# Kernel tuning notes

Hardware: AMD Instinct MI355X
Metric: run time of the kernel (lower is better)

The kernel has to match this reference:

```python
import jax, jax.numpy as jnp
import numpy as np
import math

N_ITERS = 10
N_SPIXELS = 256
NEG_INF = -1e10


def _grid_layout(h, w, n_spixels):
    # init_grid: near-square superpixel grid
    nw = int(math.sqrt(n_spixels * w / h))
    nh = int(math.sqrt(n_spixels * h / w))
    cy = np.minimum((np.arange(h) * nh) // h, nh - 1)
    cx = np.minimum((np.arange(w) * nw) // w, nw - 1)
    iy = np.broadcast_to(cy[:, None], (h, w))
    ix = np.broadcast_to(cx[None, :], (h, w))
    init_idx = iy * nw + ix  # [h,w] hard grid assignment
    # 9 candidate superpixels per pixel (3x3 neighborhood of its grid cell)
    offs = np.array([(dy, dx) for dy in (-1, 0, 1) for dx in (-1, 0, 1)])
    ny = iy[None] + offs[:, 0, None, None]  # [9,h,w]
    nx = ix[None] + offs[:, 1, None, None]
    valid = (ny >= 0) & (ny < nh) & (nx >= 0) & (nx < nw)
    nidx = np.clip(ny, 0, nh - 1) * nw + np.clip(nx, 0, nw - 1)
    return init_idx.astype(np.int32), nidx.astype(np.int32), valid, nw, nh


def setup_inputs() -> dict:
    key = jax.random.key(0)
    x = jax.random.normal(key, (2, 20, 512, 512), dtype=jnp.float32)
    return {"x": x}


def reference(x):
    b, c, h, w = x.shape
    init_idx_np, nidx_np, valid_np, nw, nh = _grid_layout(h, w, N_SPIXELS)
    K = nw * nh
    n = h * w
    init_idx = jnp.asarray(init_idx_np.reshape(n))          # [N]
    nidx = jnp.asarray(nidx_np.reshape(9, n))                # [9,N]
    valid = jnp.asarray(valid_np.reshape(9, n))              # [9,N]
    flat_nidx = nidx.reshape(-1)                             # [9N]

    pf_all = x.reshape(b, c, n)

    def init_spf(pf):  # pf [c,N] -> [c,K]: hard-assignment mean (InitSpixelFeats)
        s = jax.ops.segment_sum(pf.T, init_idx, num_segments=K)      # [K,c]
        cnt = jax.ops.segment_sum(jnp.ones((n,), pf.dtype), init_idx, num_segments=K)
        return (s / jnp.maximum(cnt, 1.0)[:, None]).T

    def calc_neg_dist(pf, spf):  # CalcAssoc: [9,N] neg sq dist to 9 neighbors
        nf = spf[:, nidx]                                    # [c,9,N]
        d = jnp.sum((pf[:, None, :] - nf) ** 2, axis=0)      # [9,N]
        return jnp.where(valid, -d, NEG_INF)

    def map_p2sp(pf, Q):  # CalcSpixelFeats: Q-weighted scatter mean, Q [9,N]
        wf = (pf[:, None, :] * Q[None]).reshape(c, -1)       # [c,9N]
        num = jax.ops.segment_sum(wf.T, flat_nidx, num_segments=K)   # [K,c]
        den = jax.ops.segment_sum(Q.reshape(-1), flat_nidx, num_segments=K)
        return (num / jnp.maximum(den, 1e-8)[:, None]).T

    def per_sample(pf):
        spf0 = init_spf(jax.lax.stop_gradient(pf))  # spf init from detached pf
        Q0 = jnp.zeros((9, n), pf.dtype)
        def body(carry, _):
            spf, _ = carry
            Q = jax.nn.softmax(calc_neg_dist(pf, spf), axis=0)
            return (map_p2sp(pf, Q), Q), None
        (spf, Q), _ = jax.lax.scan(body, (spf0, Q0), None, length=N_ITERS)
        return Q, spf

    Q, spf = jax.vmap(per_sample)(pf_all)
    return Q.reshape(b, 9, h, w), spf, x
```

## Files before the change

### kernel.cpp

```cpp
#include <hip/hip_runtime.h>

#define BATCH 2
#define C 20
#define H 512
#define W 512
#define NPIX (H*W)
#define NW 16
#define NH 16
#define K 256
#define NITERS 10
#define SPLIT 4
#define PITCH 260
#define NEG_INF_F (-1.0e10f)
#define PART_STRIDE 189

__global__ void ssn_init_kernel(const float* __restrict__ x,
                                float* __restrict__ spf0) {
    int bi = blockIdx.x;
    int ch = bi % C;
    int k  = (bi / C) % K;
    int b  = bi / (C * K);
    int ky = k >> 4, kx = k & 15;
    const float* src = x + ((size_t)(b * C + ch)) * NPIX;
    int l = threadIdx.x;
    float s = 0.f;
#pragma unroll
    for (int i = 0; i < 16; ++i) {
        int p = l + 64 * i;
        int y = ky * 32 + (p >> 5);
        int xx = kx * 32 + (p & 31);
        s += src[y * W + xx];
    }
#pragma unroll
    for (int o = 32; o > 0; o >>= 1) s += __shfl_down(s, o);
    if (l == 0) spf0[(b * K + k) * C + ch] = s * (1.0f / 1024.0f);
}

__global__ void ssn_reduce_kernel(const float* __restrict__ part,
                                  float* __restrict__ spf,
                                  float* __restrict__ outSpf,
                                  int final_mode) {
    int idx = blockIdx.x * blockDim.x + threadIdx.x;
    if (idx >= BATCH * K * C) return;
    int ch = idx % C;
    int k  = (idx / C) % K;
    int b  = idx / (C * K);
    int ky = k >> 4, kx = k & 15;
    float num = 0.f, den = 0.f;
#pragma unroll
    for (int j2 = 0; j2 < 9; ++j2) {
        int cy = ky - (j2 / 3 - 1), cx = kx - (j2 % 3 - 1);
        if (cy >= 0 && cy < NH && cx >= 0 && cx < NW) {
            const float* p = part +
                (size_t)(b * K + cy * NW + cx) * (SPLIT * PART_STRIDE) + j2 * 21;
#pragma unroll
            for (int ss = 0; ss < SPLIT; ++ss) {
                num += p[ss * PART_STRIDE + ch];
                den += p[ss * PART_STRIDE + 20];
            }
        }
    }
    float v = num / fmaxf(den, 1e-8f);
    if (final_mode) outSpf[(b * C + ch) * K + k] = v;
    else            spf[(b * K + k) * C + ch]    = v;
}

__global__ __launch_bounds__(256)
void ssn_iterate_kernel(const float* __restrict__ x,
                        const float* __restrict__ spf,
                        float* __restrict__ wpart,
                        float* __restrict__ outQ,
                        int last) {
    __shared__ float spf_lds[9][C];
    __shared__ float sumsq_lds[9];
    __shared__ float pf_tile[C][PITCH];
    __shared__ float w_tile[9][PITCH];

    int t = threadIdx.x;
    int bi = blockIdx.x;
    int s    = bi & 3;
    int cell = (bi >> 2) & (K - 1);
    int b    = bi >> 10;
    int ky = cell >> 4, kx = cell & 15;

    if (t < 9 * C) {
        int jj = t / C, ch = t % C;
        int ny = ky + jj / 3 - 1, nx = kx + jj % 3 - 1;
        float v = 0.f;
        if (ny >= 0 && ny < NH && nx >= 0 && nx < NW)
            v = spf[(size_t)(b * K + ny * NW + nx) * C + ch];
        spf_lds[jj][ch] = v;
    }
    if (t < 9) {
        int ny = ky + t / 3 - 1, nx = kx + t % 3 - 1;
        float ss2 = 0.f;
        if (ny >= 0 && ny < NH && nx >= 0 && nx < NW) {
            const float* sp = spf + (size_t)(b * K + ny * NW + nx) * C;
#pragma unroll
            for (int ch = 0; ch < C; ++ch) ss2 += sp[ch] * sp[ch];
        }
        sumsq_lds[t] = ss2;
    }
    __syncthreads();

    int py = t >> 5, px = t & 31;
    int y  = ky * 32 + s * 8 + py;
    int xx = kx * 32 + px;

    float pf[C];
    const float* xb = x + (size_t)b * C * NPIX + y * W + xx;
#pragma unroll
    for (int ch = 0; ch < C; ++ch) pf[ch] = xb[(size_t)ch * NPIX];

    float sc[9];
#pragma unroll
    for (int j = 0; j < 9; ++j) {
        int ny = ky + j / 3 - 1, nx = kx + j % 3 - 1;
        bool valid = (ny >= 0 && ny < NH && nx >= 0 && nx < NW);
        float dot = 0.f;
#pragma unroll
        for (int ch = 0; ch < C; ++ch) dot = fmaf(pf[ch], spf_lds[j][ch], dot);
        sc[j] = valid ? fmaf(2.f, dot, -sumsq_lds[j]) : NEG_INF_F;
    }
    float m = sc[0];
#pragma unroll
    for (int j = 1; j < 9; ++j) m = fmaxf(m, sc[j]);
    float wv[9], wsum = 0.f;
#pragma unroll
    for (int j = 0; j < 9; ++j) { wv[j] = __expf(sc[j] - m); wsum += wv[j]; }
    float inv = 1.0f / wsum;
#pragma unroll
    for (int j = 0; j < 9; ++j) { wv[j] *= inv; w_tile[j][t] = wv[j]; }
#pragma unroll
    for (int ch = 0; ch < C; ++ch) pf_tile[ch][t] = pf[ch];

    if (last) {
        float* q = outQ + (size_t)b * 9 * NPIX + y * W + xx;
#pragma unroll
        for (int j = 0; j < 9; ++j) q[(size_t)j * NPIX] = wv[j];
    }
    __syncthreads();

    if (t < PART_STRIDE) {
        int j = t / 21, r = t % 21;
        const float4* wt = (const float4*)&w_tile[j][0];
        float acc = 0.f;
        if (r < 20) {
            const float4* pt = (const float4*)&pf_tile[r][0];
#pragma unroll 4
            for (int p = 0; p < 64; ++p) {
                float4 w4 = wt[p];
                float4 f4 = pt[p];
                acc += w4.x * f4.x + w4.y * f4.y + w4.z * f4.z + w4.w * f4.w;
            }
        } else {
#pragma unroll 4
            for (int p = 0; p < 64; ++p) {
                float4 w4 = wt[p];
                acc += w4.x + w4.y + w4.z + w4.w;
            }
        }
        wpart[(size_t)(b * K + cell) * (SPLIT * PART_STRIDE)
              + s * PART_STRIDE + t] = acc;
    }
}

extern "C" void kernel_launch(void* const* d_in, const int* in_sizes, int n_in,
                              void* d_out, int out_size, void* d_ws, size_t ws_size,
                              hipStream_t stream) {
    const float* x = (const float*)d_in[0];
    float* out = (float*)d_out;
    float* outQ   = out;
    float* outSpf = out + (size_t)BATCH * 9 * NPIX;
    float* outX   = outSpf + (size_t)BATCH * C * K;

    float* ws   = (float*)d_ws;
    float* spf  = ws;
    float* part = spf + (size_t)BATCH * K * C;

    hipMemcpyAsync(outX, x, sizeof(float) * (size_t)BATCH * C * NPIX,
                   hipMemcpyDeviceToDevice, stream);

    ssn_init_kernel<<<BATCH * K * C, 64, 0, stream>>>(x, spf);

    for (int it = 0; it < NITERS; ++it) {
        ssn_iterate_kernel<<<BATCH * K * SPLIT, 256, 0, stream>>>(
            x, spf, part, outQ, (it == NITERS - 1) ? 1 : 0);
        if (it < NITERS - 1)
            ssn_reduce_kernel<<<(BATCH * K * C + 255) / 256, 256, 0, stream>>>(
                part, spf, nullptr, 0);
    }
    ssn_reduce_kernel<<<(BATCH * K * C + 255) / 256, 256, 0, stream>>>(
        part, nullptr, outSpf, 1);
}
```

Measured before the change: 273.1 us.

## Fuse x copy into init, register-tile the weighted scatter reduction, hoist pixel loads

```diff
diff --git a/kernel.cpp b/kernel.cpp
--- a/kernel.cpp
+++ b/kernel.cpp
@@ -14,26 +14,55 @@
 #define NEG_INF_F (-1.0e10f)
 #define PART_STRIDE 189
 
-__global__ void ssn_init_kernel(const float* __restrict__ x,
-                                float* __restrict__ spf0) {
+__global__ __launch_bounds__(256)
+void ssn_init_kernel(const float* __restrict__ x,
+                     float* __restrict__ outX,
+                     float* __restrict__ wpart) {
+    __shared__ float pf_tile[C][PITCH];
+    __shared__ float chpart[80];
+    int t = threadIdx.x;
     int bi = blockIdx.x;
-    int ch = bi % C;
-    int k  = (bi / C) % K;
-    int b  = bi / (C * K);
-    int ky = k >> 4, kx = k & 15;
-    const float* src = x + ((size_t)(b * C + ch)) * NPIX;
-    int l = threadIdx.x;
-    float s = 0.f;
-#pragma unroll
-    for (int i = 0; i < 16; ++i) {
-        int p = l + 64 * i;
-        int y = ky * 32 + (p >> 5);
-        int xx = kx * 32 + (p & 31);
-        s += src[y * W + xx];
-    }
-#pragma unroll
-    for (int o = 32; o > 0; o >>= 1) s += __shfl_down(s, o);
-    if (l == 0) spf0[(b * K + k) * C + ch] = s * (1.0f / 1024.0f);
+    int s    = bi & 3;
+    int cell = (bi >> 2) & (K - 1);
+    int b    = bi >> 10;
+    int ky = cell >> 4, kx = cell & 15;
+    int py = t >> 5, px = t & 31;
+    int y  = ky * 32 + s * 8 + py;
+    int xx = kx * 32 + px;
+
+    const float* xb = x    + (size_t)b * C * NPIX + y * W + xx;
+    float*       ox = outX + (size_t)b * C * NPIX + y * W + xx;
+#pragma unroll
+    for (int ch = 0; ch < C; ++ch) {
+        float v = xb[(size_t)ch * NPIX];
+        ox[(size_t)ch * NPIX] = v;
+        pf_tile[ch][t] = v;
+    }
+    __syncthreads();
+    if (t < 80) {
+        int ch = t >> 2, q = t & 3;
+        const float4* p = (const float4*)&pf_tile[ch][0];
+        float s4 = 0.f;
+#pragma unroll
+        for (int i = 0; i < 16; ++i) {
+            float4 v = p[q * 16 + i];
+            s4 += v.x + v.y + v.z + v.w;
+        }
+        chpart[t] = s4;
+    }
+    __syncthreads();
+    if (t < PART_STRIDE) {
+        float v = 0.f;
+        if (t >= 84 && t < 104) {
+            int ch = t - 84;
+            v = chpart[ch * 4] + chpart[ch * 4 + 1]
+              + chpart[ch * 4 + 2] + chpart[ch * 4 + 3];
+        } else if (t == 104) {
+            v = 256.0f;
+        }
+        wpart[(size_t)(b * K + cell) * (SPLIT * PART_STRIDE)
+              + s * PART_STRIDE + t] = v;
+    }
 }
 
 __global__ void ssn_reduce_kernel(const float* __restrict__ part,
@@ -73,7 +102,7 @@
                         int last) {
     __shared__ float spf_lds[9][C];
     __shared__ float sumsq_lds[9];
-    __shared__ float pf_tile[C][PITCH];
+    __shared__ float pf_tile[C + 1][PITCH];
     __shared__ float w_tile[9][PITCH];
 
     int t = threadIdx.x;
@@ -82,6 +111,15 @@
     int cell = (bi >> 2) & (K - 1);
     int b    = bi >> 10;
     int ky = cell >> 4, kx = cell & 15;
+
+    int py = t >> 5, px = t & 31;
+    int y  = ky * 32 + s * 8 + py;
+    int xx = kx * 32 + px;
+
+    float pf[C];
+    const float* xb = x + (size_t)b * C * NPIX + y * W + xx;
+#pragma unroll
+    for (int ch = 0; ch < C; ++ch) pf[ch] = xb[(size_t)ch * NPIX];
 
     if (t < 9 * C) {
         int jj = t / C, ch = t % C;
@@ -103,15 +141,6 @@
     }
     __syncthreads();
 
-    int py = t >> 5, px = t & 31;
-    int y  = ky * 32 + s * 8 + py;
-    int xx = kx * 32 + px;
-
-    float pf[C];
-    const float* xb = x + (size_t)b * C * NPIX + y * W + xx;
-#pragma unroll
-    for (int ch = 0; ch < C; ++ch) pf[ch] = xb[(size_t)ch * NPIX];
-
     float sc[9];
 #pragma unroll
     for (int j = 0; j < 9; ++j) {
@@ -133,6 +162,7 @@
     for (int j = 0; j < 9; ++j) { wv[j] *= inv; w_tile[j][t] = wv[j]; }
 #pragma unroll
     for (int ch = 0; ch < C; ++ch) pf_tile[ch][t] = pf[ch];
+    pf_tile[C][t] = 1.0f;
 
     if (last) {
         float* q = outQ + (size_t)b * 9 * NPIX + y * W + xx;
@@ -141,27 +171,53 @@
     }
     __syncthreads();
 
-    if (t < PART_STRIDE) {
-        int j = t / 21, r = t % 21;
-        const float4* wt = (const float4*)&w_tile[j][0];
-        float acc = 0.f;
-        if (r < 20) {
-            const float4* pt = (const float4*)&pf_tile[r][0];
-#pragma unroll 4
-            for (int p = 0; p < 64; ++p) {
-                float4 w4 = wt[p];
-                float4 f4 = pt[p];
-                acc += w4.x * f4.x + w4.y * f4.y + w4.z * f4.z + w4.w * f4.w;
-            }
-        } else {
-#pragma unroll 4
-            for (int p = 0; p < 64; ++p) {
-                float4 w4 = wt[p];
-                acc += w4.x + w4.y + w4.z + w4.w;
-            }
-        }
-        wpart[(size_t)(b * K + cell) * (SPLIT * PART_STRIDE)
-              + s * PART_STRIDE + t] = acc;
+    if (t < 144) {
+        int tile = t >> 4;
+        int lane = t & 15;
+        int jt = tile / 3;
+        int rt = tile % 3;
+        float acc[3][7];
+#pragma unroll
+        for (int jj = 0; jj < 3; ++jj)
+#pragma unroll
+            for (int rr = 0; rr < 7; ++rr) acc[jj][rr] = 0.f;
+
+#pragma unroll
+        for (int cc = 0; cc < 4; ++cc) {
+            int c4 = lane + (cc << 4);
+            float4 w4[3], f4[7];
+#pragma unroll
+            for (int jj = 0; jj < 3; ++jj)
+                w4[jj] = ((const float4*)&w_tile[3 * jt + jj][0])[c4];
+#pragma unroll
+            for (int rr = 0; rr < 7; ++rr)
+                f4[rr] = ((const float4*)&pf_tile[7 * rt + rr][0])[c4];
+#pragma unroll
+            for (int jj = 0; jj < 3; ++jj)
+#pragma unroll
+                for (int rr = 0; rr < 7; ++rr) {
+                    acc[jj][rr] = fmaf(w4[jj].x, f4[rr].x, acc[jj][rr]);
+                    acc[jj][rr] = fmaf(w4[jj].y, f4[rr].y, acc[jj][rr]);
+                    acc[jj][rr] = fmaf(w4[jj].z, f4[rr].z, acc[jj][rr]);
+                    acc[jj][rr] = fmaf(w4[jj].w, f4[rr].w, acc[jj][rr]);
+                }
+        }
+#pragma unroll
+        for (int off = 8; off >= 1; off >>= 1)
+#pragma unroll
+            for (int jj = 0; jj < 3; ++jj)
+#pragma unroll
+                for (int rr = 0; rr < 7; ++rr)
+                    acc[jj][rr] += __shfl_down(acc[jj][rr], off);
+        if (lane == 0) {
+            float* dst = wpart + (size_t)(b * K + cell) * (SPLIT * PART_STRIDE)
+                       + s * PART_STRIDE;
+#pragma unroll
+            for (int jj = 0; jj < 3; ++jj)
+#pragma unroll
+                for (int rr = 0; rr < 7; ++rr)
+                    dst[(3 * jt + jj) * 21 + 7 * rt + rr] = acc[jj][rr];
+        }
     }
 }
 
@@ -178,18 +234,14 @@
     float* spf  = ws;
     float* part = spf + (size_t)BATCH * K * C;
 
-    hipMemcpyAsync(outX, x, sizeof(float) * (size_t)BATCH * C * NPIX,
-                   hipMemcpyDeviceToDevice, stream);
-
-    ssn_init_kernel<<<BATCH * K * C, 64, 0, stream>>>(x, spf);
+    ssn_init_kernel<<<BATCH * K * SPLIT, 256, 0, stream>>>(x, outX, part);
+    ssn_reduce_kernel<<<160, 64, 0, stream>>>(part, spf, nullptr, 0);
 
     for (int it = 0; it < NITERS; ++it) {
         ssn_iterate_kernel<<<BATCH * K * SPLIT, 256, 0, stream>>>(
             x, spf, part, outQ, (it == NITERS - 1) ? 1 : 0);
         if (it < NITERS - 1)
-            ssn_reduce_kernel<<<(BATCH * K * C + 255) / 256, 256, 0, stream>>>(
-                part, spf, nullptr, 0);
-    }
-    ssn_reduce_kernel<<<(BATCH * K * C + 255) / 256, 256, 0, stream>>>(
-        part, nullptr, outSpf, 1);
-}
+            ssn_reduce_kernel<<<160, 64, 0, stream>>>(part, spf, nullptr, 0);
+    }
+    ssn_reduce_kernel<<<160, 64, 0, stream>>>(part, nullptr, outSpf, 1);
+}
```

After: 255.5 us. 1.07x faster.
